# Performance work log

Measured on AMD Instinct MI355X. Metric: run time of the kernel, lower is better.

## Reference

```python
import jax, jax.numpy as jnp
import numpy as np

B, L, S, D, H = 256, 256, 253, 768, 128


def setup_inputs() -> dict:
    key = jax.random.key(0)
    ks = jax.random.split(key, 11)
    sc = lambda d: 1.0 / np.sqrt(d).astype(np.float32)
    return {
        "context_embeds": jax.random.normal(ks[0], (B, L, D), jnp.float32),
        "candidate_embeds": jax.random.normal(ks[1], (B, S, D), jnp.float32),
        "ctx_mask": jax.random.randint(ks[2], (B, L), 0, 2, jnp.int32),
        "cand_mask": jax.random.randint(ks[3], (B, S), 0, 2, jnp.int32),
        "WK": jax.random.normal(ks[4], (D, D), jnp.float32) * sc(D),
        "WQ": jax.random.normal(ks[5], (D, D), jnp.float32) * sc(D),
        "WV": jax.random.normal(ks[6], (D, 1), jnp.float32) * sc(D),
        "W1": jax.random.normal(ks[7], (L, H), jnp.float32) * sc(L),
        "b1": jnp.zeros((H,), jnp.float32),
        "W2": jax.random.normal(ks[8], (H, 5), jnp.float32) * sc(H),
        "b2": jnp.zeros((5,), jnp.float32),
    }


def reference(context_embeds, candidate_embeds, ctx_mask, cand_mask,
              WK, WQ, WV, W1, b1, W2, b2):
    # Linear projections (weights stored [in, out])
    q = jnp.einsum('bld,dk->blk', context_embeds, WQ)     # [B,L,D]
    k = jnp.einsum('bsd,dk->bsk', candidate_embeds, WK)   # [B,S,D]
    v = jnp.einsum('bsd,dv->bsv', candidate_embeds, WV)   # [B,S,1]

    # attn_mask = outer product of context/candidate attention masks
    mask = (ctx_mask[:, :, None] * cand_mask[:, None, :]).astype(bool)  # [B,L,S]

    scale = 1.0 / jnp.sqrt(jnp.asarray(q.shape[-1], q.dtype))
    logits = jnp.einsum('bld,bsd->bls', q, k) * scale     # [B,L,S]
    # masked positions get bias -inf; sigmoid(-inf) = 0, so mask post-sigmoid
    attn = jnp.where(mask, jax.nn.sigmoid(logits), jnp.zeros((), logits.dtype))
    # dropout_p=0.2 is inactive (train=False default)
    x = jnp.einsum('bls,bsv->blv', attn, v)               # [B,L,1]

    xT = jnp.swapaxes(x, 1, 2)                            # [B,1,L]
    h = xT @ W1 + b1                                      # [B,1,H] (no activation)
    y = h @ W2 + b2                                       # [B,1,5]
    return y
```

## Files before the change

### kernel.cpp

```cpp
#include <hip/hip_runtime.h>
#include <hip/hip_bf16.h>
#include <stdint.h>

#define B_  256
#define L_  256
#define S_  253
#define D_  768
#define H_  128

typedef __bf16 bf16x8 __attribute__((ext_vector_type(8)));
typedef float  f32x4  __attribute__((ext_vector_type(4)));

__device__ __forceinline__ ushort f2bf(float f) {
  union { float f; uint32_t u; } v; v.f = f;
  uint32_t r = v.u + 0x7FFFu + ((v.u >> 16) & 1u);
  return (ushort)(r >> 16);
}

__device__ __forceinline__ uint32_t cvtpk(float lo, float hi) {
  uint32_t r;
  asm("v_cvt_pk_bf16_f32 %0, %1, %2" : "=v"(r) : "v"(lo), "v"(hi));
  return r;
}

__device__ __forceinline__ void gload16(const void* g, void* l) {
  __builtin_amdgcn_global_load_lds((const __attribute__((address_space(1))) void*)g,
                                   (__attribute__((address_space(3))) void*)l,
                                   16, 0, 0);
}

#define SRC_OFF(l) ((((l) & 3) ^ (((l) >> 3) & 3)) * 8)
#define RD_OFF(l)  (((((l) >> 4) ^ (((l) >> 1) & 3))) * 8)
#define PANEL128 (128 * 32)
#define PANEL256 (256 * 32 + 32)

__global__ __launch_bounds__(256) void k_cnt(const int* __restrict__ ctx_mask,
                                             int* __restrict__ cntbuf) {
  __shared__ int wsum[4];
  int b = blockIdx.x, tid = threadIdx.x;
  int m = ctx_mask[(size_t)b * 256 + tid] != 0;
  unsigned long long bal = __ballot(m);
  if ((tid & 63) == 0) wsum[tid >> 6] = __popcll(bal);
  __syncthreads();
  if (tid == 0) cntbuf[b] = wsum[0] + wsum[1] + wsum[2] + wsum[3];
}

__global__ __launch_bounds__(256) void k_scan(const int* __restrict__ cntbuf,
                                              int* __restrict__ start) {
  __shared__ int lds[256];
  int tid = threadIdx.x;
  lds[tid] = cntbuf[tid];
  __syncthreads();
  for (int off = 1; off < 256; off <<= 1) {
    int v = (tid >= off) ? lds[tid - off] : 0;
    __syncthreads();
    lds[tid] += v;
    __syncthreads();
  }
  start[tid + 1] = lds[tid];
  if (tid == 0) start[0] = 0;
}

__global__ __launch_bounds__(256) void k_scatter(const int* __restrict__ ctx_mask,
                                                 const int* __restrict__ start,
                                                 int* __restrict__ rowidx,
                                                 int* __restrict__ rowl) {
  __shared__ int lds[256];
  int b = blockIdx.x, tid = threadIdx.x;
  int m = ctx_mask[(size_t)b * 256 + tid] != 0;
  lds[tid] = m;
  __syncthreads();
  for (int off = 1; off < 256; off <<= 1) {
    int v = (tid >= off) ? lds[tid - off] : 0;
    __syncthreads();
    lds[tid] += v;
    __syncthreads();
  }
  if (m) {
    int dst = start[b] + lds[tid] - 1;
    rowidx[dst] = b * 256 + tid;
    rowl[dst]   = tid;
  }
}

__global__ __launch_bounds__(256) void k_wqb(const float* __restrict__ WQ,
                                             ushort* __restrict__ wqb) {
  int i = blockIdx.x * 256 + threadIdx.x;
  float4 c = ((const float4*)WQ)[i];
  ushort4 o;
  o.x = f2bf(c.x); o.y = f2bf(c.y); o.z = f2bf(c.z); o.w = f2bf(c.w);
  ((ushort4*)wqb)[i] = o;
}

__global__ __launch_bounds__(256) void k_mtm(const float* __restrict__ WK,
                                             const ushort* __restrict__ wqb,
                                             ushort* __restrict__ Mt) {
  const float scale = 0.03608439182435161f;
  __shared__ __align__(16) ushort As[2][PANEL128];
  __shared__ __align__(16) ushort Bs[2][PANEL128];
  int bm = blockIdx.x / 6, bn = blockIdx.x % 6;
  int row0 = bm * 128, col0 = bn * 128;
  int tid = threadIdx.x;
  int w = tid >> 6, l = tid & 63;
  int wr = w >> 1, wc = w & 1;
  int src_off = SRC_OFF(l);
  int rd_off  = RD_OFF(l);

  int rt = tid >> 4;
  int c4 = tid & 15;
  int h_thr = c4 >> 3;
  int cw = c4 & 7;
  const float* athr = WK + (size_t)(row0 + rt) * D_ + 4 * c4;
  int aw_base = rt * 64 + ((cw >> 1) ^ ((rt >> 1) & 3)) * 16 + (cw & 1) * 8;
  char* aw_ptr = (char*)&As[h_thr][0] + aw_base;

  f32x4 acc[4][4];
#pragma unroll
  for (int m = 0; m < 4; ++m)
#pragma unroll
    for (int n = 0; n < 4; ++n) acc[m][n] = (f32x4){0.f, 0.f, 0.f, 0.f};

  float4 ap0, ap1, ap2, ap3, ap4, ap5, ap6, ap7;
  ap0 = *(const float4*)(athr + 0 * 12288);
  ap1 = *(const float4*)(athr + 1 * 12288);
  ap2 = *(const float4*)(athr + 2 * 12288);
  ap3 = *(const float4*)(athr + 3 * 12288);
  ap4 = *(const float4*)(athr + 4 * 12288);
  ap5 = *(const float4*)(athr + 5 * 12288);
  ap6 = *(const float4*)(athr + 6 * 12288);
  ap7 = *(const float4*)(athr + 7 * 12288);

  for (int i = 0; i < 12; ++i) {
    int kt = i * 64;
    if (i) __syncthreads();
    {
      uint2 d;
      d.x = cvtpk(ap0.x, ap0.y); d.y = cvtpk(ap0.z, ap0.w);
      *(uint2*)(aw_ptr + 0 * 1024) = d;
      d.x = cvtpk(ap1.x, ap1.y); d.y = cvtpk(ap1.z, ap1.w);
      *(uint2*)(aw_ptr + 1 * 1024) = d;
      d.x = cvtpk(ap2.x, ap2.y); d.y = cvtpk(ap2.z, ap2.w);
      *(uint2*)(aw_ptr + 2 * 1024) = d;
      d.x = cvtpk(ap3.x, ap3.y); d.y = cvtpk(ap3.z, ap3.w);
      *(uint2*)(aw_ptr + 3 * 1024) = d;
      d.x = cvtpk(ap4.x, ap4.y); d.y = cvtpk(ap4.z, ap4.w);
      *(uint2*)(aw_ptr + 4 * 1024) = d;
      d.x = cvtpk(ap5.x, ap5.y); d.y = cvtpk(ap5.z, ap5.w);
      *(uint2*)(aw_ptr + 5 * 1024) = d;
      d.x = cvtpk(ap6.x, ap6.y); d.y = cvtpk(ap6.z, ap6.w);
      *(uint2*)(aw_ptr + 6 * 1024) = d;
      d.x = cvtpk(ap7.x, ap7.y); d.y = cvtpk(ap7.z, ap7.w);
      *(uint2*)(aw_ptr + 7 * 1024) = d;
    }
#pragma unroll
    for (int hh = 0; hh < 2; ++hh)
#pragma unroll
      for (int g = 0; g < 2; ++g) {
        int grp = w * 2 + g;
        int grow = grp * 16 + (l >> 2);
        const ushort* bsrc = wqb + (size_t)(col0 + grow) * D_ + kt + hh * 32 + src_off;
        gload16(bsrc, (char*)Bs[hh] + grp * 1024);
      }
    {
      int ktn = (i < 11) ? kt + 64 : kt;
      const float* an = athr + ktn;
      ap0 = *(const float4*)(an + 0 * 12288);
      ap1 = *(const float4*)(an + 1 * 12288);
      ap2 = *(const float4*)(an + 2 * 12288);
      ap3 = *(const float4*)(an + 3 * 12288);
      ap4 = *(const float4*)(an + 4 * 12288);
      ap5 = *(const float4*)(an + 5 * 12288);
      ap6 = *(const float4*)(an + 6 * 12288);
      ap7 = *(const float4*)(an + 7 * 12288);
    }
    __syncthreads();

#pragma unroll
    for (int hh = 0; hh < 2; ++hh) {
      bf16x8 af[4], bfr[4];
#pragma unroll
      for (int m = 0; m < 4; ++m)
        af[m] = *(const bf16x8*)&As[hh][(wr * 64 + m * 16 + (l & 15)) * 32 + rd_off];
#pragma unroll
      for (int n = 0; n < 4; ++n)
        bfr[n] = *(const bf16x8*)&Bs[hh][(wc * 64 + n * 16 + (l & 15)) * 32 + rd_off];
#pragma unroll
      for (int m = 0; m < 4; ++m)
#pragma unroll
        for (int n = 0; n < 4; ++n)
          acc[m][n] = __builtin_amdgcn_mfma_f32_16x16x32_bf16(af[m], bfr[n], acc[m][n], 0, 0, 0);
    }
  }

  int rbase = row0 + wr * 64;
  int cbase = col0 + wc * 64;
#pragma unroll
  for (int m = 0; m < 4; ++m)
#pragma unroll
    for (int n = 0; n < 4; ++n)
#pragma unroll
      for (int i = 0; i < 4; ++i) {
        int rr = rbase + m * 16 + (l >> 4) * 4 + i;
        int cc = cbase + n * 16 + (l & 15);
        Mt[(size_t)rr * D_ + cc] = f2bf(acc[m][n][i] * scale);
      }
}

__global__ __launch_bounds__(256) void k_qm(const float* __restrict__ ctx,
                                            const ushort* __restrict__ Mt,
                                            const int* __restrict__ rowidx,
                                            const int* __restrict__ start,
                                            ushort* __restrict__ qm) {
  __shared__ __align__(16) ushort As[2][PANEL128];
  __shared__ __align__(16) ushort Bs[2][PANEL128];
  int total = start[256];
  int bid0 = blockIdx.x;
  int xcd = bid0 & 7;
  int idx = bid0 >> 3;
  int bm = (idx / 6) * 8 + xcd;
  int bn = idx % 6;
  int row0 = bm * 128, col0 = bn * 128;
  if (row0 >= total) return;
  int tid = threadIdx.x;
  int w = tid >> 6, l = tid & 63;
  int wr = w >> 1, wc = w & 1;
  int src_off = SRC_OFF(l);
  int rd_off  = RD_OFF(l);

  int rt = tid >> 4;
  int c4 = tid & 15;
  int h_thr = c4 >> 3;
  int cw = c4 & 7;
  int aw_base = rt * 64 + ((cw >> 1) ^ ((rt >> 1) & 3)) * 16 + (cw & 1) * 8;
  char* aw_ptr = (char*)&As[h_thr][0] + aw_base;

  const float *apt0, *apt1, *apt2, *apt3, *apt4, *apt5, *apt6, *apt7;
  {
    int t1 = total - 1;
    int rc;
    rc = row0 + rt +   0; rc = rc < t1 ? rc : t1;
    apt0 = ctx + (size_t)rowidx[rc] * D_ + 4 * c4;
    rc = row0 + rt +  16; rc = rc < t1 ? rc : t1;
    apt1 = ctx + (size_t)rowidx[rc] * D_ + 4 * c4;
    rc = row0 + rt +  32; rc = rc < t1 ? rc : t1;
    apt2 = ctx + (size_t)rowidx[rc] * D_ + 4 * c4;
    rc = row0 + rt +  48; rc = rc < t1 ? rc : t1;
    apt3 = ctx + (size_t)rowidx[rc] * D_ + 4 * c4;
    rc = row0 + rt +  64; rc = rc < t1 ? rc : t1;
    apt4 = ctx + (size_t)rowidx[rc] * D_ + 4 * c4;
    rc = row0 + rt +  80; rc = rc < t1 ? rc : t1;
    apt5 = ctx + (size_t)rowidx[rc] * D_ + 4 * c4;
    rc = row0 + rt +  96; rc = rc < t1 ? rc : t1;
    apt6 = ctx + (size_t)rowidx[rc] * D_ + 4 * c4;
    rc = row0 + rt + 112; rc = rc < t1 ? rc : t1;
    apt7 = ctx + (size_t)rowidx[rc] * D_ + 4 * c4;
  }

  f32x4 acc[4][4];
#pragma unroll
  for (int m = 0; m < 4; ++m)
#pragma unroll
    for (int n = 0; n < 4; ++n) acc[m][n] = (f32x4){0.f, 0.f, 0.f, 0.f};

  float4 ap0, ap1, ap2, ap3, ap4, ap5, ap6, ap7;
  ap0 = *(const float4*)(apt0);
  ap1 = *(const float4*)(apt1);
  ap2 = *(const float4*)(apt2);
  ap3 = *(const float4*)(apt3);
  ap4 = *(const float4*)(apt4);
  ap5 = *(const float4*)(apt5);
  ap6 = *(const float4*)(apt6);
  ap7 = *(const float4*)(apt7);

  for (int i = 0; i < 12; ++i) {
    int kt = i * 64;
    if (i) __syncthreads();
    {
      uint2 d;
      d.x = cvtpk(ap0.x, ap0.y); d.y = cvtpk(ap0.z, ap0.w);
      *(uint2*)(aw_ptr + 0 * 1024) = d;
      d.x = cvtpk(ap1.x, ap1.y); d.y = cvtpk(ap1.z, ap1.w);
      *(uint2*)(aw_ptr + 1 * 1024) = d;
      d.x = cvtpk(ap2.x, ap2.y); d.y = cvtpk(ap2.z, ap2.w);
      *(uint2*)(aw_ptr + 2 * 1024) = d;
      d.x = cvtpk(ap3.x, ap3.y); d.y = cvtpk(ap3.z, ap3.w);
      *(uint2*)(aw_ptr + 3 * 1024) = d;
      d.x = cvtpk(ap4.x, ap4.y); d.y = cvtpk(ap4.z, ap4.w);
      *(uint2*)(aw_ptr + 4 * 1024) = d;
      d.x = cvtpk(ap5.x, ap5.y); d.y = cvtpk(ap5.z, ap5.w);
      *(uint2*)(aw_ptr + 5 * 1024) = d;
      d.x = cvtpk(ap6.x, ap6.y); d.y = cvtpk(ap6.z, ap6.w);
      *(uint2*)(aw_ptr + 6 * 1024) = d;
      d.x = cvtpk(ap7.x, ap7.y); d.y = cvtpk(ap7.z, ap7.w);
      *(uint2*)(aw_ptr + 7 * 1024) = d;
    }
#pragma unroll
    for (int hh = 0; hh < 2; ++hh)
#pragma unroll
      for (int g = 0; g < 2; ++g) {
        int grp = w * 2 + g;
        int grow = grp * 16 + (l >> 2);
        const ushort* bsrc = Mt + (size_t)(col0 + grow) * D_ + kt + hh * 32 + src_off;
        gload16(bsrc, (char*)Bs[hh] + grp * 1024);
      }
    {
      int ktn = (i < 11) ? kt + 64 : kt;
      ap0 = *(const float4*)(apt0 + ktn);
      ap1 = *(const float4*)(apt1 + ktn);
      ap2 = *(const float4*)(apt2 + ktn);
      ap3 = *(const float4*)(apt3 + ktn);
      ap4 = *(const float4*)(apt4 + ktn);
      ap5 = *(const float4*)(apt5 + ktn);
      ap6 = *(const float4*)(apt6 + ktn);
      ap7 = *(const float4*)(apt7 + ktn);
    }
    __syncthreads();

#pragma unroll
    for (int hh = 0; hh < 2; ++hh) {
      bf16x8 af[4], bfr[4];
#pragma unroll
      for (int m = 0; m < 4; ++m)
        af[m] = *(const bf16x8*)&As[hh][(wr * 64 + m * 16 + (l & 15)) * 32 + rd_off];
#pragma unroll
      for (int n = 0; n < 4; ++n)
        bfr[n] = *(const bf16x8*)&Bs[hh][(wc * 64 + n * 16 + (l & 15)) * 32 + rd_off];
#pragma unroll
      for (int m = 0; m < 4; ++m)
#pragma unroll
        for (int n = 0; n < 4; ++n)
          acc[m][n] = __builtin_amdgcn_mfma_f32_16x16x32_bf16(af[m], bfr[n], acc[m][n], 0, 0, 0);
    }
  }

  int rbase = row0 + wr * 64;
  int cbase = col0 + wc * 64;
#pragma unroll
  for (int m = 0; m < 4; ++m)
#pragma unroll
    for (int n = 0; n < 4; ++n)
#pragma unroll
      for (int i = 0; i < 4; ++i) {
        int rr = rbase + m * 16 + (l >> 4) * 4 + i;
        int cc = cbase + n * 16 + (l & 15);
        if (rr < total) qm[(size_t)rr * D_ + cc] = f2bf(acc[m][n][i]);
      }
}

__global__ __launch_bounds__(1024) void k_attn(const ushort* __restrict__ qm,
                                               const float* __restrict__ cand,
                                               const int* __restrict__ cand_mask,
                                               const int* __restrict__ start,
                                               const int* __restrict__ rowl,
                                               const float* __restrict__ WV,
                                               float* __restrict__ xbuf) {
  __shared__ __align__(16) ushort As[4][PANEL256];
  __shared__ __align__(16) ushort Bs[4][PANEL256];
  __shared__ float wv_lds[D_];
  __shared__ float w_lds[256];
  __shared__ float xpart[4][256];
  int b = blockIdx.x;
  int st = start[b];
  int cnt = start[b + 1] - st;
  int total = start[256];
  int tid = threadIdx.x;
  int w = tid >> 6, l = tid & 63;
  int wr = w >> 2, wc = w & 3;
  int src_off = SRC_OFF(l);
  int rd_off  = RD_OFF(l);

  if (tid < D_) wv_lds[tid] = WV[tid];

  int rt = tid >> 4;
  int c4 = tid & 15;
  int h_thr = c4 >> 3;
  int cw = c4 & 7;
  int row_k0 = rt, row_k1 = rt + 64, row_k2 = rt + 128, row_k3 = rt + 192;
  int ok3 = row_k3 < S_;
  const float* bptr0 = cand + ((size_t)b * S_ + row_k0) * D_ + 4 * c4;
  const float* bptr1 = cand + ((size_t)b * S_ + row_k1) * D_ + 4 * c4;
  const float* bptr2 = cand + ((size_t)b * S_ + row_k2) * D_ + 4 * c4;
  const float* bptr3 = cand + ((size_t)b * S_ + (ok3 ? row_k3 : S_ - 1)) * D_ + 4 * c4;
  int bw_base = rt * 64 + ((cw >> 1) ^ ((rt >> 1) & 3)) * 16 + (cw & 1) * 8;

  int arow_l = st + w * 16 + (l >> 2);
  arow_l = arow_l < total ? arow_l : total - 1;
  const ushort* aptr = qm + (size_t)arow_l * D_ + src_off;

  f32x4 acc[4][4];
#pragma unroll
  for (int m = 0; m < 4; ++m)
#pragma unroll
    for (int n = 0; n < 4; ++n) acc[m][n] = (f32x4){0.f, 0.f, 0.f, 0.f};
  float wa0 = 0.f, wa1 = 0.f, wa2 = 0.f, wa3 = 0.f;

  __syncthreads();

  float4 bp0 = *(const float4*)(bptr0);
  float4 bp1 = *(const float4*)(bptr1);
  float4 bp2 = *(const float4*)(bptr2);
  float4 bp3 = *(const float4*)(bptr3);
  if (!ok3) bp3 = (float4){0.f, 0.f, 0.f, 0.f};

  {
    char* bw_ptr = (char*)&Bs[h_thr][0] + bw_base;
    uint2 d;
    d.x = cvtpk(bp0.x, bp0.y); d.y = cvtpk(bp0.z, bp0.w);
    *(uint2*)(bw_ptr + 0 * 4096) = d;
    d.x = cvtpk(bp1.x, bp1.y); d.y = cvtpk(bp1.z, bp1.w);
    *(uint2*)(bw_ptr + 1 * 4096) = d;
    d.x = cvtpk(bp2.x, bp2.y); d.y = cvtpk(bp2.z, bp2.w);
    *(uint2*)(bw_ptr + 2 * 4096) = d;
    d.x = cvtpk(bp3.x, bp3.y); d.y = cvtpk(bp3.z, bp3.w);
    *(uint2*)(bw_ptr + 3 * 4096) = d;
#pragma unroll
    for (int h = 0; h < 2; ++h)
      gload16(aptr + h * 32, (char*)As[h] + w * 1024);
    float4 wv = *(const float4*)&wv_lds[4 * c4];
    wa0 += bp0.x * wv.x + bp0.y * wv.y + bp0.z * wv.z + bp0.w * wv.w;
    wa1 += bp1.x * wv.x + bp1.y * wv.y + bp1.z * wv.z + bp1.w * wv.w;
    wa2 += bp2.x * wv.x + bp2.y * wv.y + bp2.z * wv.z + bp2.w * wv.w;
    wa3 += bp3.x * wv.x + bp3.y * wv.y + bp3.z * wv.z + bp3.w * wv.w;
    bp0 = *(const float4*)(bptr0 + 64);
    bp1 = *(const float4*)(bptr1 + 64);
    bp2 = *(const float4*)(bptr2 + 64);
    bp3 = *(const float4*)(bptr3 + 64);
    if (!ok3) bp3 = (float4){0.f, 0.f, 0.f, 0.f};
  }
  __syncthreads();

  for (int i = 0; i < 12; ++i) {
    int cur = i & 1, nxt = cur ^ 1;
    if (i < 11) {
      int ktn = (i + 1) * 64;
      char* bw_ptr = (char*)&Bs[nxt * 2 + h_thr][0] + bw_base;
      uint2 d;
      d.x = cvtpk(bp0.x, bp0.y); d.y = cvtpk(bp0.z, bp0.w);
      *(uint2*)(bw_ptr + 0 * 4096) = d;
      d.x = cvtpk(bp1.x, bp1.y); d.y = cvtpk(bp1.z, bp1.w);
      *(uint2*)(bw_ptr + 1 * 4096) = d;
      d.x = cvtpk(bp2.x, bp2.y); d.y = cvtpk(bp2.z, bp2.w);
      *(uint2*)(bw_ptr + 2 * 4096) = d;
      d.x = cvtpk(bp3.x, bp3.y); d.y = cvtpk(bp3.z, bp3.w);
      *(uint2*)(bw_ptr + 3 * 4096) = d;
#pragma unroll
      for (int h = 0; h < 2; ++h)
        gload16(aptr + ktn + h * 32, (char*)As[nxt * 2 + h] + w * 1024);
      float4 wv = *(const float4*)&wv_lds[ktn + 4 * c4];
      wa0 += bp0.x * wv.x + bp0.y * wv.y + bp0.z * wv.z + bp0.w * wv.w;
      wa1 += bp1.x * wv.x + bp1.y * wv.y + bp1.z * wv.z + bp1.w * wv.w;
      wa2 += bp2.x * wv.x + bp2.y * wv.y + bp2.z * wv.z + bp2.w * wv.w;
      wa3 += bp3.x * wv.x + bp3.y * wv.y + bp3.z * wv.z + bp3.w * wv.w;
      if (i < 10) {
        int ktn2 = ktn + 64;
        bp0 = *(const float4*)(bptr0 + ktn2);
        bp1 = *(const float4*)(bptr1 + ktn2);
        bp2 = *(const float4*)(bptr2 + ktn2);
        bp3 = *(const float4*)(bptr3 + ktn2);
        if (!ok3) bp3 = (float4){0.f, 0.f, 0.f, 0.f};
      }
    }
#pragma unroll
    for (int h = 0; h < 2; ++h) {
      bf16x8 af[4], bfr[4];
#pragma unroll
      for (int m = 0; m < 4; ++m)
        af[m] = *(const bf16x8*)&As[cur * 2 + h][(wr * 64 + m * 16 + (l & 15)) * 32 + rd_off];
#pragma unroll
      for (int n = 0; n < 4; ++n)
        bfr[n] = *(const bf16x8*)&Bs[cur * 2 + h][(wc * 64 + n * 16 + (l & 15)) * 32 + rd_off];
#pragma unroll
      for (int m = 0; m < 4; ++m)
#pragma unroll
        for (int n = 0; n < 4; ++n)
          acc[m][n] = __builtin_amdgcn_mfma_f32_16x16x32_bf16(af[m], bfr[n], acc[m][n], 0, 0, 0);
    }
    __syncthreads();
  }

  wa0 += __shfl_xor(wa0, 1, 64); wa0 += __shfl_xor(wa0, 2, 64);
  wa0 += __shfl_xor(wa0, 4, 64); wa0 += __shfl_xor(wa0, 8, 64);
  wa1 += __shfl_xor(wa1, 1, 64); wa1 += __shfl_xor(wa1, 2, 64);
  wa1 += __shfl_xor(wa1, 4, 64); wa1 += __shfl_xor(wa1, 8, 64);
  wa2 += __shfl_xor(wa2, 1, 64); wa2 += __shfl_xor(wa2, 2, 64);
  wa2 += __shfl_xor(wa2, 4, 64); wa2 += __shfl_xor(wa2, 8, 64);
  wa3 += __shfl_xor(wa3, 1, 64); wa3 += __shfl_xor(wa3, 2, 64);
  wa3 += __shfl_xor(wa3, 4, 64); wa3 += __shfl_xor(wa3, 8, 64);
  if (c4 == 0) {
    const int* cm = cand_mask + (size_t)b * S_;
    w_lds[row_k0] = (cm[row_k0] != 0) ? wa0 : 0.f;
    w_lds[row_k1] = (cm[row_k1] != 0) ? wa1 : 0.f;
    w_lds[row_k2] = (cm[row_k2] != 0) ? wa2 : 0.f;
    w_lds[row_k3] = (ok3 && cm[ok3 ? row_k3 : 0] != 0) ? wa3 : 0.f;
  }
  __syncthreads();

  float rs[4][4];
#pragma unroll
  for (int m = 0; m < 4; ++m)
#pragma unroll
    for (int i = 0; i < 4; ++i) rs[m][i] = 0.f;

#pragma unroll
  for (int n = 0; n < 4; ++n) {
    float wcol = w_lds[wc * 64 + n * 16 + (l & 15)];
#pragma unroll
    for (int m = 0; m < 4; ++m)
#pragma unroll
      for (int i = 0; i < 4; ++i) {
        float p = 1.f / (1.f + __expf(-acc[m][n][i]));
        rs[m][i] += p * wcol;
      }
  }
#pragma unroll
  for (int m = 0; m < 4; ++m)
#pragma unroll
    for (int i = 0; i < 4; ++i) {
      float v = rs[m][i];
      v += __shfl_xor(v, 1, 64);
      v += __shfl_xor(v, 2, 64);
      v += __shfl_xor(v, 4, 64);
      v += __shfl_xor(v, 8, 64);
      rs[m][i] = v;
    }
  if ((l & 15) == 0) {
#pragma unroll
    for (int m = 0; m < 4; ++m)
#pragma unroll
      for (int i = 0; i < 4; ++i)
        xpart[wc][wr * 64 + m * 16 + (l >> 4) * 4 + i] = rs[m][i];
  }
  __syncthreads();
  if (tid < 256) {
    float xs = xpart[0][tid] + xpart[1][tid] + xpart[2][tid] + xpart[3][tid];
    xbuf[(size_t)b * 256 + tid] = 0.f;
    __syncthreads();
    if (tid < cnt)
      xbuf[(size_t)b * 256 + rowl[st + tid]] = xs;
  } else {
    __syncthreads();
  }
}

__global__ __launch_bounds__(128) void k_mlp(const float* __restrict__ xbuf,
                                             const float* __restrict__ W1,
                                             const float* __restrict__ b1,
                                             const float* __restrict__ W2,
                                             const float* __restrict__ b2,
                                             float* __restrict__ out) {
  int b = blockIdx.x, t = threadIdx.x;
  __shared__ float xl[256];
  __shared__ float hl[128];
  xl[t]       = xbuf[(size_t)b * 256 + t];
  xl[t + 128] = xbuf[(size_t)b * 256 + 128 + t];
  __syncthreads();
  float acc = b1[t];
#pragma unroll 8
  for (int ll = 0; ll < 256; ++ll) acc += xl[ll] * W1[ll * H_ + t];
  hl[t] = acc;
  __syncthreads();
  if (t < 5) {
    float y = b2[t];
#pragma unroll 8
    for (int h = 0; h < H_; ++h) y += hl[h] * W2[h * 5 + t];
    out[(size_t)b * 5 + t] = y;
  }
}

extern "C" void kernel_launch(void* const* d_in, const int* in_sizes, int n_in,
                              void* d_out, int out_size, void* d_ws, size_t ws_size,
                              hipStream_t stream) {
  const float* ctx       = (const float*)d_in[0];
  const float* cand      = (const float*)d_in[1];
  const int*   ctx_mask  = (const int*)d_in[2];
  const int*   cand_mask = (const int*)d_in[3];
  const float* WK        = (const float*)d_in[4];
  const float* WQ        = (const float*)d_in[5];
  const float* WV        = (const float*)d_in[6];
  const float* W1        = (const float*)d_in[7];
  const float* b1        = (const float*)d_in[8];
  const float* W2        = (const float*)d_in[9];
  const float* b2        = (const float*)d_in[10];
  float* out = (float*)d_out;

  char* ws = (char*)d_ws;
  size_t off = 0;
  auto alloc = [&](size_t bytes) {
    void* p = ws + off;
    off += (bytes + 255) & ~(size_t)255;
    return p;
  };
  ushort* Mt     = (ushort*)alloc((size_t)D_ * D_ * 2);
  ushort* wqb    = (ushort*)alloc((size_t)D_ * D_ * 2);
  float*  xbuf   = (float*) alloc((size_t)B_ * L_ * 4);
  int*    cntbuf = (int*)   alloc(256 * 4);
  int*    startb = (int*)   alloc(257 * 4);
  int*    rowidx = (int*)   alloc((size_t)B_ * L_ * 4);
  int*    rowlb  = (int*)   alloc((size_t)B_ * L_ * 4);
  ushort* qm     = (ushort*)alloc((size_t)B_ * L_ * D_ * 2);
  (void)ws_size; (void)in_sizes; (void)n_in; (void)out_size;

  k_cnt    <<<B_,                256, 0, stream>>>(ctx_mask, cntbuf);
  k_scan   <<<1,                 256, 0, stream>>>(cntbuf, startb);
  k_scatter<<<B_,                256, 0, stream>>>(ctx_mask, startb, rowidx, rowlb);
  k_wqb    <<<D_ * D_ / 4 / 256, 256, 0, stream>>>(WQ, wqb);
  k_mtm    <<<36,                256, 0, stream>>>(WK, wqb, Mt);
  k_qm     <<<B_ * L_ / 128 * 6, 256, 0, stream>>>(ctx, Mt, rowidx, startb, qm);
  k_attn   <<<B_,               1024, 0, stream>>>(qm, cand, cand_mask, startb, rowlb, WV, xbuf);
  k_mlp    <<<B_,                128, 0, stream>>>(xbuf, W1, b1, W2, b2, out);
}
```

Baseline: 194.3 us.

## Compact masked candidate rows in attention and compute M with scalar FP32 kernel

```diff
diff --git a/kernel.cpp b/kernel.cpp
--- a/kernel.cpp
+++ b/kernel.cpp
@@ -83,23 +83,67 @@
   }
 }
 
-__global__ __launch_bounds__(256) void k_wqb(const float* __restrict__ WQ,
-                                             ushort* __restrict__ wqb) {
-  int i = blockIdx.x * 256 + threadIdx.x;
-  float4 c = ((const float4*)WQ)[i];
-  ushort4 o;
-  o.x = f2bf(c.x); o.y = f2bf(c.y); o.z = f2bf(c.z); o.w = f2bf(c.w);
-  ((ushort4*)wqb)[i] = o;
-}
-
-__global__ __launch_bounds__(256) void k_mtm(const float* __restrict__ WK,
-                                             const ushort* __restrict__ wqb,
-                                             ushort* __restrict__ Mt) {
+__global__ __launch_bounds__(256) void k_scat_s(const int* __restrict__ cand_mask,
+                                                int* __restrict__ crowidx,
+                                                int* __restrict__ cnts) {
+  __shared__ int lds[256];
+  int b = blockIdx.x, tid = threadIdx.x;
+  int m = (tid < S_) ? (cand_mask[(size_t)b * S_ + tid] != 0) : 0;
+  lds[tid] = m;
+  __syncthreads();
+  for (int off = 1; off < 256; off <<= 1) {
+    int v = (tid >= off) ? lds[tid - off] : 0;
+    __syncthreads();
+    lds[tid] += v;
+    __syncthreads();
+  }
+  if (m) crowidx[(size_t)b * 256 + lds[tid] - 1] = tid;
+  if (tid == 255) cnts[b] = lds[255];
+}
+
+__global__ __launch_bounds__(256) void k_mt(const float* __restrict__ WK,
+                                            const float* __restrict__ WQ,
+                                            ushort* __restrict__ Mt) {
   const float scale = 0.03608439182435161f;
+  int bid = blockIdx.x;
+  int i0 = (bid / 3) * 4;
+  int j  = (bid % 3) * 256 + threadIdx.x;
+  const float4* wq  = (const float4*)(WQ + (size_t)j * D_);
+  const float4* wk0 = (const float4*)(WK + (size_t)(i0 + 0) * D_);
+  const float4* wk1 = (const float4*)(WK + (size_t)(i0 + 1) * D_);
+  const float4* wk2 = (const float4*)(WK + (size_t)(i0 + 2) * D_);
+  const float4* wk3 = (const float4*)(WK + (size_t)(i0 + 3) * D_);
+  float a0 = 0.f, a1 = 0.f, a2 = 0.f, a3 = 0.f;
+#pragma unroll 4
+  for (int t = 0; t < D_ / 4; ++t) {
+    float4 q = wq[t];
+    float4 k0 = wk0[t], k1 = wk1[t], k2 = wk2[t], k3 = wk3[t];
+    a0 += q.x * k0.x + q.y * k0.y + q.z * k0.z + q.w * k0.w;
+    a1 += q.x * k1.x + q.y * k1.y + q.z * k1.z + q.w * k1.w;
+    a2 += q.x * k2.x + q.y * k2.y + q.z * k2.z + q.w * k2.w;
+    a3 += q.x * k3.x + q.y * k3.y + q.z * k3.z + q.w * k3.w;
+  }
+  Mt[(size_t)(i0 + 0) * D_ + j] = f2bf(a0 * scale);
+  Mt[(size_t)(i0 + 1) * D_ + j] = f2bf(a1 * scale);
+  Mt[(size_t)(i0 + 2) * D_ + j] = f2bf(a2 * scale);
+  Mt[(size_t)(i0 + 3) * D_ + j] = f2bf(a3 * scale);
+}
+
+__global__ __launch_bounds__(256) void k_qm(const float* __restrict__ ctx,
+                                            const ushort* __restrict__ Mt,
+                                            const int* __restrict__ rowidx,
+                                            const int* __restrict__ start,
+                                            ushort* __restrict__ qm) {
   __shared__ __align__(16) ushort As[2][PANEL128];
   __shared__ __align__(16) ushort Bs[2][PANEL128];
-  int bm = blockIdx.x / 6, bn = blockIdx.x % 6;
+  int total = start[256];
+  int bid0 = blockIdx.x;
+  int xcd = bid0 & 7;
+  int idx = bid0 >> 3;
+  int bm = (idx / 6) * 8 + xcd;
+  int bn = idx % 6;
   int row0 = bm * 128, col0 = bn * 128;
+  if (row0 >= total) return;
   int tid = threadIdx.x;
   int w = tid >> 6, l = tid & 63;
   int wr = w >> 1, wc = w & 1;
@@ -110,10 +154,31 @@
   int c4 = tid & 15;
   int h_thr = c4 >> 3;
   int cw = c4 & 7;
-  const float* athr = WK + (size_t)(row0 + rt) * D_ + 4 * c4;
   int aw_base = rt * 64 + ((cw >> 1) ^ ((rt >> 1) & 3)) * 16 + (cw & 1) * 8;
   char* aw_ptr = (char*)&As[h_thr][0] + aw_base;
 
+  const float *apt0, *apt1, *apt2, *apt3, *apt4, *apt5, *apt6, *apt7;
+  {
+    int t1 = total - 1;
+    int rc;
+    rc = row0 + rt +   0; rc = rc < t1 ? rc : t1;
+    apt0 = ctx + (size_t)rowidx[rc] * D_ + 4 * c4;
+    rc = row0 + rt +  16; rc = rc < t1 ? rc : t1;
+    apt1 = ctx + (size_t)rowidx[rc] * D_ + 4 * c4;
+    rc = row0 + rt +  32; rc = rc < t1 ? rc : t1;
+    apt2 = ctx + (size_t)rowidx[rc] * D_ + 4 * c4;
+    rc = row0 + rt +  48; rc = rc < t1 ? rc : t1;
+    apt3 = ctx + (size_t)rowidx[rc] * D_ + 4 * c4;
+    rc = row0 + rt +  64; rc = rc < t1 ? rc : t1;
+    apt4 = ctx + (size_t)rowidx[rc] * D_ + 4 * c4;
+    rc = row0 + rt +  80; rc = rc < t1 ? rc : t1;
+    apt5 = ctx + (size_t)rowidx[rc] * D_ + 4 * c4;
+    rc = row0 + rt +  96; rc = rc < t1 ? rc : t1;
+    apt6 = ctx + (size_t)rowidx[rc] * D_ + 4 * c4;
+    rc = row0 + rt + 112; rc = rc < t1 ? rc : t1;
+    apt7 = ctx + (size_t)rowidx[rc] * D_ + 4 * c4;
+  }
+
   f32x4 acc[4][4];
 #pragma unroll
   for (int m = 0; m < 4; ++m)
@@ -121,14 +186,14 @@
     for (int n = 0; n < 4; ++n) acc[m][n] = (f32x4){0.f, 0.f, 0.f, 0.f};
 
   float4 ap0, ap1, ap2, ap3, ap4, ap5, ap6, ap7;
-  ap0 = *(const float4*)(athr + 0 * 12288);
-  ap1 = *(const float4*)(athr + 1 * 12288);
-  ap2 = *(const float4*)(athr + 2 * 12288);
-  ap3 = *(const float4*)(athr + 3 * 12288);
-  ap4 = *(const float4*)(athr + 4 * 12288);
-  ap5 = *(const float4*)(athr + 5 * 12288);
-  ap6 = *(const float4*)(athr + 6 * 12288);
-  ap7 = *(const float4*)(athr + 7 * 12288);
+  ap0 = *(const float4*)(apt0);
+  ap1 = *(const float4*)(apt1);
+  ap2 = *(const float4*)(apt2);
+  ap3 = *(const float4*)(apt3);
+  ap4 = *(const float4*)(apt4);
+  ap5 = *(const float4*)(apt5);
+  ap6 = *(const float4*)(apt6);
+  ap7 = *(const float4*)(apt7);
 
   for (int i = 0; i < 12; ++i) {
     int kt = i * 64;
@@ -158,148 +223,6 @@
       for (int g = 0; g < 2; ++g) {
         int grp = w * 2 + g;
         int grow = grp * 16 + (l >> 2);
-        const ushort* bsrc = wqb + (size_t)(col0 + grow) * D_ + kt + hh * 32 + src_off;
-        gload16(bsrc, (char*)Bs[hh] + grp * 1024);
-      }
-    {
-      int ktn = (i < 11) ? kt + 64 : kt;
-      const float* an = athr + ktn;
-      ap0 = *(const float4*)(an + 0 * 12288);
-      ap1 = *(const float4*)(an + 1 * 12288);
-      ap2 = *(const float4*)(an + 2 * 12288);
-      ap3 = *(const float4*)(an + 3 * 12288);
-      ap4 = *(const float4*)(an + 4 * 12288);
-      ap5 = *(const float4*)(an + 5 * 12288);
-      ap6 = *(const float4*)(an + 6 * 12288);
-      ap7 = *(const float4*)(an + 7 * 12288);
-    }
-    __syncthreads();
-
-#pragma unroll
-    for (int hh = 0; hh < 2; ++hh) {
-      bf16x8 af[4], bfr[4];
-#pragma unroll
-      for (int m = 0; m < 4; ++m)
-        af[m] = *(const bf16x8*)&As[hh][(wr * 64 + m * 16 + (l & 15)) * 32 + rd_off];
-#pragma unroll
-      for (int n = 0; n < 4; ++n)
-        bfr[n] = *(const bf16x8*)&Bs[hh][(wc * 64 + n * 16 + (l & 15)) * 32 + rd_off];
-#pragma unroll
-      for (int m = 0; m < 4; ++m)
-#pragma unroll
-        for (int n = 0; n < 4; ++n)
-          acc[m][n] = __builtin_amdgcn_mfma_f32_16x16x32_bf16(af[m], bfr[n], acc[m][n], 0, 0, 0);
-    }
-  }
-
-  int rbase = row0 + wr * 64;
-  int cbase = col0 + wc * 64;
-#pragma unroll
-  for (int m = 0; m < 4; ++m)
-#pragma unroll
-    for (int n = 0; n < 4; ++n)
-#pragma unroll
-      for (int i = 0; i < 4; ++i) {
-        int rr = rbase + m * 16 + (l >> 4) * 4 + i;
-        int cc = cbase + n * 16 + (l & 15);
-        Mt[(size_t)rr * D_ + cc] = f2bf(acc[m][n][i] * scale);
-      }
-}
-
-__global__ __launch_bounds__(256) void k_qm(const float* __restrict__ ctx,
-                                            const ushort* __restrict__ Mt,
-                                            const int* __restrict__ rowidx,
-                                            const int* __restrict__ start,
-                                            ushort* __restrict__ qm) {
-  __shared__ __align__(16) ushort As[2][PANEL128];
-  __shared__ __align__(16) ushort Bs[2][PANEL128];
-  int total = start[256];
-  int bid0 = blockIdx.x;
-  int xcd = bid0 & 7;
-  int idx = bid0 >> 3;
-  int bm = (idx / 6) * 8 + xcd;
-  int bn = idx % 6;
-  int row0 = bm * 128, col0 = bn * 128;
-  if (row0 >= total) return;
-  int tid = threadIdx.x;
-  int w = tid >> 6, l = tid & 63;
-  int wr = w >> 1, wc = w & 1;
-  int src_off = SRC_OFF(l);
-  int rd_off  = RD_OFF(l);
-
-  int rt = tid >> 4;
-  int c4 = tid & 15;
-  int h_thr = c4 >> 3;
-  int cw = c4 & 7;
-  int aw_base = rt * 64 + ((cw >> 1) ^ ((rt >> 1) & 3)) * 16 + (cw & 1) * 8;
-  char* aw_ptr = (char*)&As[h_thr][0] + aw_base;
-
-  const float *apt0, *apt1, *apt2, *apt3, *apt4, *apt5, *apt6, *apt7;
-  {
-    int t1 = total - 1;
-    int rc;
-    rc = row0 + rt +   0; rc = rc < t1 ? rc : t1;
-    apt0 = ctx + (size_t)rowidx[rc] * D_ + 4 * c4;
-    rc = row0 + rt +  16; rc = rc < t1 ? rc : t1;
-    apt1 = ctx + (size_t)rowidx[rc] * D_ + 4 * c4;
-    rc = row0 + rt +  32; rc = rc < t1 ? rc : t1;
-    apt2 = ctx + (size_t)rowidx[rc] * D_ + 4 * c4;
-    rc = row0 + rt +  48; rc = rc < t1 ? rc : t1;
-    apt3 = ctx + (size_t)rowidx[rc] * D_ + 4 * c4;
-    rc = row0 + rt +  64; rc = rc < t1 ? rc : t1;
-    apt4 = ctx + (size_t)rowidx[rc] * D_ + 4 * c4;
-    rc = row0 + rt +  80; rc = rc < t1 ? rc : t1;
-    apt5 = ctx + (size_t)rowidx[rc] * D_ + 4 * c4;
-    rc = row0 + rt +  96; rc = rc < t1 ? rc : t1;
-    apt6 = ctx + (size_t)rowidx[rc] * D_ + 4 * c4;
-    rc = row0 + rt + 112; rc = rc < t1 ? rc : t1;
-    apt7 = ctx + (size_t)rowidx[rc] * D_ + 4 * c4;
-  }
-
-  f32x4 acc[4][4];
-#pragma unroll
-  for (int m = 0; m < 4; ++m)
-#pragma unroll
-    for (int n = 0; n < 4; ++n) acc[m][n] = (f32x4){0.f, 0.f, 0.f, 0.f};
-
-  float4 ap0, ap1, ap2, ap3, ap4, ap5, ap6, ap7;
-  ap0 = *(const float4*)(apt0);
-  ap1 = *(const float4*)(apt1);
-  ap2 = *(const float4*)(apt2);
-  ap3 = *(const float4*)(apt3);
-  ap4 = *(const float4*)(apt4);
-  ap5 = *(const float4*)(apt5);
-  ap6 = *(const float4*)(apt6);
-  ap7 = *(const float4*)(apt7);
-
-  for (int i = 0; i < 12; ++i) {
-    int kt = i * 64;
-    if (i) __syncthreads();
-    {
-      uint2 d;
-      d.x = cvtpk(ap0.x, ap0.y); d.y = cvtpk(ap0.z, ap0.w);
-      *(uint2*)(aw_ptr + 0 * 1024) = d;
-      d.x = cvtpk(ap1.x, ap1.y); d.y = cvtpk(ap1.z, ap1.w);
-      *(uint2*)(aw_ptr + 1 * 1024) = d;
-      d.x = cvtpk(ap2.x, ap2.y); d.y = cvtpk(ap2.z, ap2.w);
-      *(uint2*)(aw_ptr + 2 * 1024) = d;
-      d.x = cvtpk(ap3.x, ap3.y); d.y = cvtpk(ap3.z, ap3.w);
-      *(uint2*)(aw_ptr + 3 * 1024) = d;
-      d.x = cvtpk(ap4.x, ap4.y); d.y = cvtpk(ap4.z, ap4.w);
-      *(uint2*)(aw_ptr + 4 * 1024) = d;
-      d.x = cvtpk(ap5.x, ap5.y); d.y = cvtpk(ap5.z, ap5.w);
-      *(uint2*)(aw_ptr + 5 * 1024) = d;
-      d.x = cvtpk(ap6.x, ap6.y); d.y = cvtpk(ap6.z, ap6.w);
-      *(uint2*)(aw_ptr + 6 * 1024) = d;
-      d.x = cvtpk(ap7.x, ap7.y); d.y = cvtpk(ap7.z, ap7.w);
-      *(uint2*)(aw_ptr + 7 * 1024) = d;
-    }
-#pragma unroll
-    for (int hh = 0; hh < 2; ++hh)
-#pragma unroll
-      for (int g = 0; g < 2; ++g) {
-        int grp = w * 2 + g;
-        int grow = grp * 16 + (l >> 2);
         const ushort* bsrc = Mt + (size_t)(col0 + grow) * D_ + kt + hh * 32 + src_off;
         gload16(bsrc, (char*)Bs[hh] + grp * 1024);
       }
@@ -349,7 +272,8 @@
 
 __global__ __launch_bounds__(1024) void k_attn(const ushort* __restrict__ qm,
                                                const float* __restrict__ cand,
-                                               const int* __restrict__ cand_mask,
+                                               const int* __restrict__ crowidx,
+                                               const int* __restrict__ cnts,
                                                const int* __restrict__ start,
                                                const int* __restrict__ rowl,
                                                const float* __restrict__ WV,
@@ -363,6 +287,8 @@
   int st = start[b];
   int cnt = start[b + 1] - st;
   int total = start[256];
+  int cs = cnts[b]; cs = cs > 1 ? cs : 1;
+  int nact = (cs + 63) >> 6;
   int tid = threadIdx.x;
   int w = tid >> 6, l = tid & 63;
   int wr = w >> 2, wc = w & 3;
@@ -375,12 +301,16 @@
   int c4 = tid & 15;
   int h_thr = c4 >> 3;
   int cw = c4 & 7;
-  int row_k0 = rt, row_k1 = rt + 64, row_k2 = rt + 128, row_k3 = rt + 192;
-  int ok3 = row_k3 < S_;
-  const float* bptr0 = cand + ((size_t)b * S_ + row_k0) * D_ + 4 * c4;
-  const float* bptr1 = cand + ((size_t)b * S_ + row_k1) * D_ + 4 * c4;
-  const float* bptr2 = cand + ((size_t)b * S_ + row_k2) * D_ + 4 * c4;
-  const float* bptr3 = cand + ((size_t)b * S_ + (ok3 ? row_k3 : S_ - 1)) * D_ + 4 * c4;
+  int j0 = rt, j1 = rt + 64, j2 = rt + 128, j3 = rt + 192;
+  const int* cri = crowidx + (size_t)b * 256;
+  int s0 = cri[j0 < cs ? j0 : cs - 1];
+  int s1 = cri[j1 < cs ? j1 : cs - 1];
+  int s2 = cri[j2 < cs ? j2 : cs - 1];
+  int s3 = cri[j3 < cs ? j3 : cs - 1];
+  const float* bptr0 = cand + ((size_t)b * S_ + s0) * D_ + 4 * c4;
+  const float* bptr1 = cand + ((size_t)b * S_ + s1) * D_ + 4 * c4;
+  const float* bptr2 = cand + ((size_t)b * S_ + s2) * D_ + 4 * c4;
+  const float* bptr3 = cand + ((size_t)b * S_ + s3) * D_ + 4 * c4;
   int bw_base = rt * 64 + ((cw >> 1) ^ ((rt >> 1) & 3)) * 16 + (cw & 1) * 8;
 
   int arow_l = st + w * 16 + (l >> 2);
@@ -400,7 +330,6 @@
   float4 bp1 = *(const float4*)(bptr1);
   float4 bp2 = *(const float4*)(bptr2);
   float4 bp3 = *(const float4*)(bptr3);
-  if (!ok3) bp3 = (float4){0.f, 0.f, 0.f, 0.f};
 
   {
     char* bw_ptr = (char*)&Bs[h_thr][0] + bw_base;
@@ -425,7 +354,6 @@
     bp1 = *(const float4*)(bptr1 + 64);
     bp2 = *(const float4*)(bptr2 + 64);
     bp3 = *(const float4*)(bptr3 + 64);
-    if (!ok3) bp3 = (float4){0.f, 0.f, 0.f, 0.f};
   }
   __syncthreads();
 
@@ -457,23 +385,24 @@
         bp1 = *(const float4*)(bptr1 + ktn2);
         bp2 = *(const float4*)(bptr2 + ktn2);
         bp3 = *(const float4*)(bptr3 + ktn2);
-        if (!ok3) bp3 = (float4){0.f, 0.f, 0.f, 0.f};
       }
     }
-#pragma unroll
-    for (int h = 0; h < 2; ++h) {
-      bf16x8 af[4], bfr[4];
-#pragma unroll
-      for (int m = 0; m < 4; ++m)
-        af[m] = *(const bf16x8*)&As[cur * 2 + h][(wr * 64 + m * 16 + (l & 15)) * 32 + rd_off];
-#pragma unroll
-      for (int n = 0; n < 4; ++n)
-        bfr[n] = *(const bf16x8*)&Bs[cur * 2 + h][(wc * 64 + n * 16 + (l & 15)) * 32 + rd_off];
-#pragma unroll
-      for (int m = 0; m < 4; ++m)
+    if (wc < nact) {
+#pragma unroll
+      for (int h = 0; h < 2; ++h) {
+        bf16x8 af[4], bfr[4];
+#pragma unroll
+        for (int m = 0; m < 4; ++m)
+          af[m] = *(const bf16x8*)&As[cur * 2 + h][(wr * 64 + m * 16 + (l & 15)) * 32 + rd_off];
 #pragma unroll
         for (int n = 0; n < 4; ++n)
-          acc[m][n] = __builtin_amdgcn_mfma_f32_16x16x32_bf16(af[m], bfr[n], acc[m][n], 0, 0, 0);
+          bfr[n] = *(const bf16x8*)&Bs[cur * 2 + h][(wc * 64 + n * 16 + (l & 15)) * 32 + rd_off];
+#pragma unroll
+        for (int m = 0; m < 4; ++m)
+#pragma unroll
+          for (int n = 0; n < 4; ++n)
+            acc[m][n] = __builtin_amdgcn_mfma_f32_16x16x32_bf16(af[m], bfr[n], acc[m][n], 0, 0, 0);
+      }
     }
     __syncthreads();
   }
@@ -487,11 +416,10 @@
   wa3 += __shfl_xor(wa3, 1, 64); wa3 += __shfl_xor(wa3, 2, 64);
   wa3 += __shfl_xor(wa3, 4, 64); wa3 += __shfl_xor(wa3, 8, 64);
   if (c4 == 0) {
-    const int* cm = cand_mask + (size_t)b * S_;
-    w_lds[row_k0] = (cm[row_k0] != 0) ? wa0 : 0.f;
-    w_lds[row_k1] = (cm[row_k1] != 0) ? wa1 : 0.f;
-    w_lds[row_k2] = (cm[row_k2] != 0) ? wa2 : 0.f;
-    w_lds[row_k3] = (ok3 && cm[ok3 ? row_k3 : 0] != 0) ? wa3 : 0.f;
+    w_lds[j0] = (j0 < cs) ? wa0 : 0.f;
+    w_lds[j1] = (j1 < cs) ? wa1 : 0.f;
+    w_lds[j2] = (j2 < cs) ? wa2 : 0.f;
+    w_lds[j3] = (j3 < cs) ? wa3 : 0.f;
   }
   __syncthreads();
 
@@ -590,22 +518,23 @@
     off += (bytes + 255) & ~(size_t)255;
     return p;
   };
-  ushort* Mt     = (ushort*)alloc((size_t)D_ * D_ * 2);
-  ushort* wqb    = (ushort*)alloc((size_t)D_ * D_ * 2);
-  float*  xbuf   = (float*) alloc((size_t)B_ * L_ * 4);
-  int*    cntbuf = (int*)   alloc(256 * 4);
-  int*    startb = (int*)   alloc(257 * 4);
-  int*    rowidx = (int*)   alloc((size_t)B_ * L_ * 4);
-  int*    rowlb  = (int*)   alloc((size_t)B_ * L_ * 4);
-  ushort* qm     = (ushort*)alloc((size_t)B_ * L_ * D_ * 2);
+  ushort* Mt      = (ushort*)alloc((size_t)D_ * D_ * 2);
+  float*  xbuf    = (float*) alloc((size_t)B_ * L_ * 4);
+  int*    cntbuf  = (int*)   alloc(256 * 4);
+  int*    startb  = (int*)   alloc(257 * 4);
+  int*    rowidx  = (int*)   alloc((size_t)B_ * L_ * 4);
+  int*    rowlb   = (int*)   alloc((size_t)B_ * L_ * 4);
+  int*    crowidx = (int*)   alloc((size_t)B_ * 256 * 4);
+  int*    cnts    = (int*)   alloc(256 * 4);
+  ushort* qm      = (ushort*)alloc((size_t)B_ * L_ * D_ * 2);
   (void)ws_size; (void)in_sizes; (void)n_in; (void)out_size;
 
   k_cnt    <<<B_,                256, 0, stream>>>(ctx_mask, cntbuf);
   k_scan   <<<1,                 256, 0, stream>>>(cntbuf, startb);
   k_scatter<<<B_,                256, 0, stream>>>(ctx_mask, startb, rowidx, rowlb);
-  k_wqb    <<<D_ * D_ / 4 / 256, 256, 0, stream>>>(WQ, wqb);
-  k_mtm    <<<36,                256, 0, stream>>>(WK, wqb, Mt);
+  k_scat_s <<<B_,                256, 0, stream>>>(cand_mask, crowidx, cnts);
+  k_mt     <<<(D_ / 4) * 3,      256, 0, stream>>>(WK, WQ, Mt);
   k_qm     <<<B_ * L_ / 128 * 6, 256, 0, stream>>>(ctx, Mt, rowidx, startb, qm);
-  k_attn   <<<B_,               1024, 0, stream>>>(qm, cand, cand_mask, startb, rowlb, WV, xbuf);
+  k_attn   <<<B_,               1024, 0, stream>>>(qm, cand, crowidx, cnts, startb, rowlb, WV, xbuf);
   k_mlp    <<<B_,                128, 0, stream>>>(xbuf, W1, b1, W2, b2, out);
 }
```

Measured after the change: 277.0 us. +42.5%, slower.
